# Kernel tuning notes

Measured on AMD Instinct MI355X. Metric: run time of the kernel, lower is better.

Reference implementation:

```python
import jax, jax.numpy as jnp
import numpy as np

SEQ_LEN = 256
NLAYERS = 3
H = 128  # latent_dim == input_dim
OUT_DIM = 2
BATCH = 1024


def setup_inputs() -> dict:
    key = jax.random.key(0)
    ks = jax.random.split(key, 7)
    s = 1.0 / np.sqrt(H)  # PyTorch RNN init scale
    return {
        "hiddens": jax.random.normal(ks[0], (BATCH, NLAYERS, H), jnp.float32),
        "W_ih": jax.random.uniform(ks[1], (NLAYERS, 3 * H, H), jnp.float32, -s, s),
        "W_hh": jax.random.uniform(ks[2], (NLAYERS, 3 * H, H), jnp.float32, -s, s),
        "b_ih": jax.random.uniform(ks[3], (NLAYERS, 3 * H), jnp.float32, -s, s),
        "b_hh": jax.random.uniform(ks[4], (NLAYERS, 3 * H), jnp.float32, -s, s),
        "fc_w": jax.random.uniform(ks[5], (OUT_DIM, H), jnp.float32, -s, s),
        "fc_b": jax.random.uniform(ks[6], (OUT_DIM,), jnp.float32, -s, s),
    }


def _gru_cell(x, h, w_ih, w_hh, bi, bh):
    # x, h: [B, H]; w_*: [3H, H]; b_*: [3H]; PyTorch gate order (r, z, n)
    gx = x @ w_ih.T + bi          # [B, 3H]
    gh = h @ w_hh.T + bh          # [B, 3H]
    xr, xz, xn = jnp.split(gx, 3, axis=-1)
    hr, hz, hn = jnp.split(gh, 3, axis=-1)
    r = jax.nn.sigmoid(xr + hr)
    z = jax.nn.sigmoid(xz + hz)
    n = jnp.tanh(xn + r * hn)
    return (1.0 - z) * n + z * h


def reference(hiddens, W_ih, W_hh, b_ih, b_hh, fc_w, fc_b):
    # hiddens: [B, L, H] -> layer-major [L, B, H] (torch transposes 0,1)
    h = jnp.transpose(hiddens, (1, 0, 2))
    B = hiddens.shape[0]
    x0 = jnp.zeros((B, H), hiddens.dtype)  # torch.zeros initial input

    def step(carry, _):
        x, h = carry
        new_h = []
        inp = x
        for l in range(NLAYERS):
            hl = _gru_cell(inp, h[l], W_ih[l], W_hh[l], b_ih[l], b_hh[l])
            new_h.append(hl)
            inp = hl  # top-layer output feeds next layer / next step
        return (inp, jnp.stack(new_h)), inp

    (_, _), outs = jax.lax.scan(step, (x0, h), None, length=SEQ_LEN)
    outs = jnp.transpose(outs, (1, 0, 2))        # [B, T, H]
    return outs @ fc_w.T + fc_b                  # [B, T, out_dim]
```

## Files before the change

kernel.cpp:

```cpp
#include <hip/hip_runtime.h>
#include <stdint.h>

typedef int   v4i __attribute__((ext_vector_type(4)));
typedef float v4f __attribute__((ext_vector_type(4)));

#define SLOT_SZ  13824
#define LO_OFF   6912
#define BIAS_OFF (2*SLOT_SZ)
#define FC_OFF   (BIAS_OFF + 6144)
#define SMEM_SZ  (FC_OFF + 2048)

#define QW   1436.84056f
#define C1f  4.38394754e-5f
#define C2f  3.45193507e-7f

__device__ __forceinline__ float sigm(float x) {
  return __builtin_amdgcn_rcpf(1.f + __expf(-x));
}
__device__ __forceinline__ float tanh_(float x) {
  return 1.f - 2.f * __builtin_amdgcn_rcpf(1.f + __expf(2.f * x));
}

__global__ void prep_weights(const float* __restrict__ Wih,
                             const float* __restrict__ Whh,
                             int8_t* __restrict__ img) {
  int bid = blockIdx.x, lane = threadIdx.x;
  int w = bid / 36, blk = bid % 36;
  int l = blk / 12, rem = blk % 12, o = rem >> 1, kh = rem & 1;
  const float* M = (o & 1) ? Whh : Wih;
  int row = (o >> 1) * 128 + w * 16 + (lane & 15);
  int k0 = kh * 64 + (lane >> 4) * 16;
  const float* src = M + l * 49152 + row * 128 + k0;
  int words[4];
  #pragma unroll
  for (int j4 = 0; j4 < 4; ++j4) {
    unsigned wd = 0;
    #pragma unroll
    for (int j = 0; j < 4; ++j) {
      int q = (int)rintf(src[j4 * 4 + j] * QW);
      wd |= ((unsigned)(q & 255)) << (8 * j);
    }
    words[j4] = (int)wd;
  }
  *(v4i*)(img + (((long)bid) * 64 + lane) * 16) = *(const v4i*)words;
}

__device__ __forceinline__ unsigned pack_hi(const float* f, const float* fhi) {
  unsigned wd = 0;
  #pragma unroll
  for (int r = 0; r < 4; ++r) {
    int v = (int)fhi[r];
    wd |= ((unsigned)(v & 255)) << (8 * r);
  }
  return wd;
}

__global__ __launch_bounds__(512, 2)
void gru_main(const float* __restrict__ hiddens, const float* __restrict__ bih,
              const float* __restrict__ bhh, const float* __restrict__ fcw,
              const float* __restrict__ fcb, const int8_t* __restrict__ img,
              float* __restrict__ out) {
  extern __shared__ char smem[];
  const int tid = threadIdx.x, wg = blockIdx.x;
  const int lane = tid & 63, w = tid >> 6, col = lane & 15, q = lane >> 4;

  v4i wr[36];
  #pragma unroll
  for (int i = 0; i < 36; ++i)
    wr[i] = *(const v4i*)(img + (((long)(w * 36 + i)) * 64 + lane) * 16);

  if (tid < 128) {
    int kh = tid >> 6, ln = tid & 63, c2 = ln & 15, q2 = ln >> 4;
    int words[4] = {0, 0, 0, 0};
    if (c2 < 2) {
      const float* src = fcw + c2 * 128 + kh * 64 + q2 * 16;
      #pragma unroll
      for (int j4 = 0; j4 < 4; ++j4) {
        unsigned wd = 0;
        #pragma unroll
        for (int j = 0; j < 4; ++j) {
          int qv = (int)rintf(src[j4 * 4 + j] * QW);
          wd |= ((unsigned)(qv & 255)) << (8 * j);
        }
        words[j4] = (int)wd;
      }
    }
    *(v4i*)(smem + FC_OFF + kh * 1024 + ln * 16) = *(const v4i*)words;
  }
  for (int i = tid; i < 1536; i += 512) {
    int l = i >> 9, type = (i >> 7) & 3, h = i & 127;
    float bv;
    if      (type == 0) bv = bih[l * 384 + h]       + bhh[l * 384 + h];
    else if (type == 1) bv = bih[l * 384 + 128 + h] + bhh[l * 384 + 128 + h];
    else if (type == 2) bv = bih[l * 384 + 256 + h];
    else                bv = bhh[l * 384 + 256 + h];
    *(float*)(smem + BIAS_OFF + i * 4) = bv;
  }
  for (int i = tid; i < 6144; i += 512) {
    int l = i >> 11, b = (i >> 7) & 15, h = i & 127;
    float v = hiddens[((long)(wg * 16 + b)) * 384 + l * 128 + h];
    float f = v * 15.875f, fhi = rintf(f);
    *(int8_t*)(smem + l * 2304 + b * 144 + h)          = (int8_t)(int)fhi;
    *(int8_t*)(smem + l * 2304 + b * 144 + h + LO_OFF) = (int8_t)(int)rintf((f - fhi) * 127.f);
  }
  v4f hst[3];
  #pragma unroll
  for (int l = 0; l < 3; ++l)
    #pragma unroll
    for (int r = 0; r < 4; ++r)
      hst[l][r] = hiddens[((long)(wg * 16 + col)) * 384 + l * 128 + w * 16 + q * 4 + r];

  const float fcb0 = fcb[0], fcb1 = fcb[1];
  __syncthreads();

  const char* fragb = smem + col * 144 + q * 16;
  char* ewb = smem + col * 144 + w * 16 + q * 4;
  const char* biasb = smem + BIAS_OFF + (w * 16 + q * 4) * 4;

  v4i c2h[2], c2l[2];

  #pragma unroll 1
  for (int t = 0; t < 256; ++t) {
    const int so = (t & 1) * SLOT_SZ;
    const int sn = SLOT_SZ - so;
    #pragma unroll
    for (int l = 0; l < 3; ++l) {
      v4i aRh = {0,0,0,0}, aRl = {0,0,0,0}, aZh = {0,0,0,0}, aZl = {0,0,0,0};
      v4i aXh = {0,0,0,0}, aXl = {0,0,0,0}, aHh = {0,0,0,0}, aHl = {0,0,0,0};
      if (l > 0 || t > 0) {
        #pragma unroll
        for (int kh = 0; kh < 2; ++kh) {
          v4i xh, xl;
          if (l == 0) {
            xh = *(const v4i*)(fragb + so + 2 * 2304 + kh * 64);
            xl = *(const v4i*)(fragb + so + 2 * 2304 + kh * 64 + LO_OFF);
            c2h[kh] = xh; c2l[kh] = xl;
          } else {
            xh = *(const v4i*)(fragb + sn + (l - 1) * 2304 + kh * 64);
            xl = *(const v4i*)(fragb + sn + (l - 1) * 2304 + kh * 64 + LO_OFF);
          }
          aRh = __builtin_amdgcn_mfma_i32_16x16x64_i8(wr[l*12 + 0 + kh], xh, aRh, 0, 0, 0);
          aRl = __builtin_amdgcn_mfma_i32_16x16x64_i8(wr[l*12 + 0 + kh], xl, aRl, 0, 0, 0);
          aZh = __builtin_amdgcn_mfma_i32_16x16x64_i8(wr[l*12 + 4 + kh], xh, aZh, 0, 0, 0);
          aZl = __builtin_amdgcn_mfma_i32_16x16x64_i8(wr[l*12 + 4 + kh], xl, aZl, 0, 0, 0);
          aXh = __builtin_amdgcn_mfma_i32_16x16x64_i8(wr[l*12 + 8 + kh], xh, aXh, 0, 0, 0);
          aXl = __builtin_amdgcn_mfma_i32_16x16x64_i8(wr[l*12 + 8 + kh], xl, aXl, 0, 0, 0);
        }
      }
      #pragma unroll
      for (int kh = 0; kh < 2; ++kh) {
        v4i hh, hl;
        if (l == 2) {
          if (t == 0) { c2h[kh] = *(const v4i*)(fragb + so + 2 * 2304 + kh * 64);
                        c2l[kh] = *(const v4i*)(fragb + so + 2 * 2304 + kh * 64 + LO_OFF); }
          hh = c2h[kh]; hl = c2l[kh];
        } else {
          hh = *(const v4i*)(fragb + so + l * 2304 + kh * 64);
          hl = *(const v4i*)(fragb + so + l * 2304 + kh * 64 + LO_OFF);
        }
        aRh = __builtin_amdgcn_mfma_i32_16x16x64_i8(wr[l*12 + 2 + kh], hh, aRh, 0, 0, 0);
        aRl = __builtin_amdgcn_mfma_i32_16x16x64_i8(wr[l*12 + 2 + kh], hl, aRl, 0, 0, 0);
        aZh = __builtin_amdgcn_mfma_i32_16x16x64_i8(wr[l*12 + 6 + kh], hh, aZh, 0, 0, 0);
        aZl = __builtin_amdgcn_mfma_i32_16x16x64_i8(wr[l*12 + 6 + kh], hl, aZl, 0, 0, 0);
        aHh = __builtin_amdgcn_mfma_i32_16x16x64_i8(wr[l*12 + 10 + kh], hh, aHh, 0, 0, 0);
        aHl = __builtin_amdgcn_mfma_i32_16x16x64_i8(wr[l*12 + 10 + kh], hl, aHl, 0, 0, 0);
      }
      v4f bRv = *(const v4f*)(biasb + (l * 4 + 0) * 512);
      v4f bZv = *(const v4f*)(biasb + (l * 4 + 1) * 512);
      v4f bXv = *(const v4f*)(biasb + (l * 4 + 2) * 512);
      v4f bHv = *(const v4f*)(biasb + (l * 4 + 3) * 512);
      unsigned hiw = 0, low = 0;
      #pragma unroll
      for (int r = 0; r < 4; ++r) {
        float gR = bRv[r] + C1f * (float)aRh[r] + C2f * (float)aRl[r];
        float gZ = bZv[r] + C1f * (float)aZh[r] + C2f * (float)aZl[r];
        float gX = bXv[r] + C1f * (float)aXh[r] + C2f * (float)aXl[r];
        float gH = bHv[r] + C1f * (float)aHh[r] + C2f * (float)aHl[r];
        float rg = sigm(gR), zg = sigm(gZ);
        float ng = tanh_(gX + rg * gH);
        float hn = ng + zg * (hst[l][r] - ng);
        hst[l][r] = hn;
        float f = hn * 15.875f, fhi = rintf(f);
        hiw |= ((unsigned)(((int)fhi) & 255)) << (8 * r);
        low |= ((unsigned)(((int)rintf((f - fhi) * 127.f)) & 255)) << (8 * r);
      }
      *(unsigned*)(ewb + sn + l * 2304)          = hiw;
      *(unsigned*)(ewb + sn + l * 2304 + LO_OFF) = low;
      __syncthreads();
    }
    if (w == 0) {
      v4i dh = {0,0,0,0}, dl = {0,0,0,0};
      #pragma unroll
      for (int kh = 0; kh < 2; ++kh) {
        v4i xh = *(const v4i*)(fragb + sn + 2 * 2304 + kh * 64);
        v4i xl = *(const v4i*)(fragb + sn + 2 * 2304 + kh * 64 + LO_OFF);
        v4i fw = *(const v4i*)(smem + FC_OFF + kh * 1024 + lane * 16);
        dh = __builtin_amdgcn_mfma_i32_16x16x64_i8(fw, xh, dh, 0, 0, 0);
        dl = __builtin_amdgcn_mfma_i32_16x16x64_i8(fw, xl, dl, 0, 0, 0);
      }
      if (q == 0) {
        float2 o2;
        o2.x = fcb0 + C1f * (float)dh[0] + C2f * (float)dl[0];
        o2.y = fcb1 + C1f * (float)dh[1] + C2f * (float)dl[1];
        *(float2*)(out + (((long)(wg * 16 + col)) * 256 + t) * 2) = o2;
      }
    }
  }
}

extern "C" void kernel_launch(void* const* d_in, const int* in_sizes, int n_in,
                              void* d_out, int out_size, void* d_ws, size_t ws_size,
                              hipStream_t stream) {
  (void)in_sizes; (void)n_in; (void)out_size; (void)ws_size;
  const float* hiddens = (const float*)d_in[0];
  const float* Wih     = (const float*)d_in[1];
  const float* Whh     = (const float*)d_in[2];
  const float* bih     = (const float*)d_in[3];
  const float* bhh     = (const float*)d_in[4];
  const float* fcw     = (const float*)d_in[5];
  const float* fcb     = (const float*)d_in[6];
  int8_t* img = (int8_t*)d_ws;
  float* out = (float*)d_out;

  prep_weights<<<288, 64, 0, stream>>>(Wih, Whh, img);
  gru_main<<<64, 512, SMEM_SZ, stream>>>(hiddens, bih, bhh, fcw, fcb, img, out);
}
```

Baseline: 900.6 us.

## Defer FC projection into next step's layer-0 phase and issue recurrent MFMAs first

Moves the wave-0 FC output projection for step t-1 into step t's layer-0 block, where it reuses the already-loaded top-layer fragments. This removes the serial FC tail that previously ran after the last barrier of each step. The final step's output is written after the loop from slot 0. Each layer now loads all operands up front and issues the hidden-state MFMAs before the input MFMAs, so MFMA work can start while input fragments arrive. The cost is more code to maintain and a new epilogue whose correctness depends on the slot parity of the final step.

```diff
diff --git a/kernel.cpp b/kernel.cpp
--- a/kernel.cpp
+++ b/kernel.cpp
@@ -45,15 +45,21 @@
   *(v4i*)(img + (((long)bid) * 64 + lane) * 16) = *(const v4i*)words;
 }
 
-__device__ __forceinline__ unsigned pack_hi(const float* f, const float* fhi) {
-  unsigned wd = 0;
-  #pragma unroll
-  for (int r = 0; r < 4; ++r) {
-    int v = (int)fhi[r];
-    wd |= ((unsigned)(v & 255)) << (8 * r);
-  }
-  return wd;
-}
+#define MFMA8(kh, Ah, Al, base)                                                \
+  aRh = __builtin_amdgcn_mfma_i32_16x16x64_i8(wr[(base) + 0 + (kh)], Ah, aRh, 0, 0, 0); \
+  aRl = __builtin_amdgcn_mfma_i32_16x16x64_i8(wr[(base) + 0 + (kh)], Al, aRl, 0, 0, 0); \
+  aZh = __builtin_amdgcn_mfma_i32_16x16x64_i8(wr[(base) + 4 + (kh)], Ah, aZh, 0, 0, 0); \
+  aZl = __builtin_amdgcn_mfma_i32_16x16x64_i8(wr[(base) + 4 + (kh)], Al, aZl, 0, 0, 0);
+
+#define MFMAX(kh, Ah, Al, base)                                                \
+  MFMA8(kh, Ah, Al, base)                                                      \
+  aXh = __builtin_amdgcn_mfma_i32_16x16x64_i8(wr[(base) + 8 + (kh)], Ah, aXh, 0, 0, 0); \
+  aXl = __builtin_amdgcn_mfma_i32_16x16x64_i8(wr[(base) + 8 + (kh)], Al, aXl, 0, 0, 0);
+
+#define MFMAH(kh, Ah, Al, base)                                                \
+  MFMA8(kh, Ah, Al, (base) + 2)                                                \
+  aHh = __builtin_amdgcn_mfma_i32_16x16x64_i8(wr[(base) + 10 + (kh)], Ah, aHh, 0, 0, 0); \
+  aHl = __builtin_amdgcn_mfma_i32_16x16x64_i8(wr[(base) + 10 + (kh)], Al, aHl, 0, 0, 0);
 
 __global__ __launch_bounds__(512, 2)
 void gru_main(const float* __restrict__ hiddens, const float* __restrict__ bih,
@@ -117,93 +123,122 @@
   char* ewb = smem + col * 144 + w * 16 + q * 4;
   const char* biasb = smem + BIAS_OFF + (w * 16 + q * 4) * 4;
 
-  v4i c2h[2], c2l[2];
+#define EW_STORE(l)                                                            \
+  {                                                                            \
+    v4f bRv = *(const v4f*)(biasb + ((l) * 4 + 0) * 512);                      \
+    v4f bZv = *(const v4f*)(biasb + ((l) * 4 + 1) * 512);                      \
+    v4f bXv = *(const v4f*)(biasb + ((l) * 4 + 2) * 512);                      \
+    v4f bHv = *(const v4f*)(biasb + ((l) * 4 + 3) * 512);                      \
+    unsigned hiw = 0, low = 0;                                                 \
+    _Pragma("unroll")                                                          \
+    for (int r = 0; r < 4; ++r) {                                              \
+      float gR = bRv[r] + C1f * (float)aRh[r] + C2f * (float)aRl[r];           \
+      float gZ = bZv[r] + C1f * (float)aZh[r] + C2f * (float)aZl[r];           \
+      float gX = bXv[r] + C1f * (float)aXh[r] + C2f * (float)aXl[r];           \
+      float gH = bHv[r] + C1f * (float)aHh[r] + C2f * (float)aHl[r];           \
+      float rg = sigm(gR), zg = sigm(gZ);                                      \
+      float ng = tanh_(gX + rg * gH);                                          \
+      float hn = ng + zg * (hst[l][r] - ng);                                   \
+      hst[l][r] = hn;                                                          \
+      float f = hn * 15.875f, fhi = rintf(f);                                  \
+      hiw |= ((unsigned)(((int)fhi) & 255)) << (8 * r);                        \
+      low |= ((unsigned)(((int)rintf((f - fhi) * 127.f)) & 255)) << (8 * r);   \
+    }                                                                          \
+    *(unsigned*)(ewb + sn + (l) * 2304)          = hiw;                        \
+    *(unsigned*)(ewb + sn + (l) * 2304 + LO_OFF) = low;                        \
+  }
 
   #pragma unroll 1
   for (int t = 0; t < 256; ++t) {
     const int so = (t & 1) * SLOT_SZ;
     const int sn = SLOT_SZ - so;
-    #pragma unroll
-    for (int l = 0; l < 3; ++l) {
+
+    {
+      v4i xh0[2], xl0[2], hh[2], hl[2];
+      #pragma unroll
+      for (int kh = 0; kh < 2; ++kh) {
+        xh0[kh] = *(const v4i*)(fragb + so + 2 * 2304 + kh * 64);
+        xl0[kh] = *(const v4i*)(fragb + so + 2 * 2304 + kh * 64 + LO_OFF);
+        hh[kh]  = *(const v4i*)(fragb + so + kh * 64);
+        hl[kh]  = *(const v4i*)(fragb + so + kh * 64 + LO_OFF);
+      }
       v4i aRh = {0,0,0,0}, aRl = {0,0,0,0}, aZh = {0,0,0,0}, aZl = {0,0,0,0};
       v4i aXh = {0,0,0,0}, aXl = {0,0,0,0}, aHh = {0,0,0,0}, aHl = {0,0,0,0};
-      if (l > 0 || t > 0) {
+      #pragma unroll
+      for (int kh = 0; kh < 2; ++kh) { MFMAH(kh, hh[kh], hl[kh], 0) }
+      if (t > 0) {
         #pragma unroll
-        for (int kh = 0; kh < 2; ++kh) {
-          v4i xh, xl;
-          if (l == 0) {
-            xh = *(const v4i*)(fragb + so + 2 * 2304 + kh * 64);
-            xl = *(const v4i*)(fragb + so + 2 * 2304 + kh * 64 + LO_OFF);
-            c2h[kh] = xh; c2l[kh] = xl;
-          } else {
-            xh = *(const v4i*)(fragb + sn + (l - 1) * 2304 + kh * 64);
-            xl = *(const v4i*)(fragb + sn + (l - 1) * 2304 + kh * 64 + LO_OFF);
+        for (int kh = 0; kh < 2; ++kh) { MFMAX(kh, xh0[kh], xl0[kh], 0) }
+        if (w == 0) {
+          v4i dh = {0,0,0,0}, dl = {0,0,0,0};
+          #pragma unroll
+          for (int kh = 0; kh < 2; ++kh) {
+            v4i fw = *(const v4i*)(smem + FC_OFF + kh * 1024 + lane * 16);
+            dh = __builtin_amdgcn_mfma_i32_16x16x64_i8(fw, xh0[kh], dh, 0, 0, 0);
+            dl = __builtin_amdgcn_mfma_i32_16x16x64_i8(fw, xl0[kh], dl, 0, 0, 0);
           }
-          aRh = __builtin_amdgcn_mfma_i32_16x16x64_i8(wr[l*12 + 0 + kh], xh, aRh, 0, 0, 0);
-          aRl = __builtin_amdgcn_mfma_i32_16x16x64_i8(wr[l*12 + 0 + kh], xl, aRl, 0, 0, 0);
-          aZh = __builtin_amdgcn_mfma_i32_16x16x64_i8(wr[l*12 + 4 + kh], xh, aZh, 0, 0, 0);
-          aZl = __builtin_amdgcn_mfma_i32_16x16x64_i8(wr[l*12 + 4 + kh], xl, aZl, 0, 0, 0);
-          aXh = __builtin_amdgcn_mfma_i32_16x16x64_i8(wr[l*12 + 8 + kh], xh, aXh, 0, 0, 0);
-          aXl = __builtin_amdgcn_mfma_i32_16x16x64_i8(wr[l*12 + 8 + kh], xl, aXl, 0, 0, 0);
+          if (q == 0) {
+            float2 o2;
+            o2.x = fcb0 + C1f * (float)dh[0] + C2f * (float)dl[0];
+            o2.y = fcb1 + C1f * (float)dh[1] + C2f * (float)dl[1];
+            *(float2*)(out + (((long)(wg * 16 + col)) * 256 + (t - 1)) * 2) = o2;
+          }
         }
       }
+      EW_STORE(0)
+    }
+    __syncthreads();
+
+    {
+      v4i xh[2], xl[2], hh[2], hl[2];
       #pragma unroll
       for (int kh = 0; kh < 2; ++kh) {
-        v4i hh, hl;
-        if (l == 2) {
-          if (t == 0) { c2h[kh] = *(const v4i*)(fragb + so + 2 * 2304 + kh * 64);
-                        c2l[kh] = *(const v4i*)(fragb + so + 2 * 2304 + kh * 64 + LO_OFF); }
-          hh = c2h[kh]; hl = c2l[kh];
-        } else {
-          hh = *(const v4i*)(fragb + so + l * 2304 + kh * 64);
-          hl = *(const v4i*)(fragb + so + l * 2304 + kh * 64 + LO_OFF);
-        }
-        aRh = __builtin_amdgcn_mfma_i32_16x16x64_i8(wr[l*12 + 2 + kh], hh, aRh, 0, 0, 0);
-        aRl = __builtin_amdgcn_mfma_i32_16x16x64_i8(wr[l*12 + 2 + kh], hl, aRl, 0, 0, 0);
-        aZh = __builtin_amdgcn_mfma_i32_16x16x64_i8(wr[l*12 + 6 + kh], hh, aZh, 0, 0, 0);
-        aZl = __builtin_amdgcn_mfma_i32_16x16x64_i8(wr[l*12 + 6 + kh], hl, aZl, 0, 0, 0);
-        aHh = __builtin_amdgcn_mfma_i32_16x16x64_i8(wr[l*12 + 10 + kh], hh, aHh, 0, 0, 0);
-        aHl = __builtin_amdgcn_mfma_i32_16x16x64_i8(wr[l*12 + 10 + kh], hl, aHl, 0, 0, 0);
-      }
-      v4f bRv = *(const v4f*)(biasb + (l * 4 + 0) * 512);
-      v4f bZv = *(const v4f*)(biasb + (l * 4 + 1) * 512);
-      v4f bXv = *(const v4f*)(biasb + (l * 4 + 2) * 512);
-      v4f bHv = *(const v4f*)(biasb + (l * 4 + 3) * 512);
-      unsigned hiw = 0, low = 0;
-      #pragma unroll
-      for (int r = 0; r < 4; ++r) {
-        float gR = bRv[r] + C1f * (float)aRh[r] + C2f * (float)aRl[r];
-        float gZ = bZv[r] + C1f * (float)aZh[r] + C2f * (float)aZl[r];
-        float gX = bXv[r] + C1f * (float)aXh[r] + C2f * (float)aXl[r];
-        float gH = bHv[r] + C1f * (float)aHh[r] + C2f * (float)aHl[r];
-        float rg = sigm(gR), zg = sigm(gZ);
-        float ng = tanh_(gX + rg * gH);
-        float hn = ng + zg * (hst[l][r] - ng);
-        hst[l][r] = hn;
-        float f = hn * 15.875f, fhi = rintf(f);
-        hiw |= ((unsigned)(((int)fhi) & 255)) << (8 * r);
-        low |= ((unsigned)(((int)rintf((f - fhi) * 127.f)) & 255)) << (8 * r);
-      }
-      *(unsigned*)(ewb + sn + l * 2304)          = hiw;
-      *(unsigned*)(ewb + sn + l * 2304 + LO_OFF) = low;
-      __syncthreads();
-    }
-    if (w == 0) {
-      v4i dh = {0,0,0,0}, dl = {0,0,0,0};
+        xh[kh] = *(const v4i*)(fragb + sn + kh * 64);
+        xl[kh] = *(const v4i*)(fragb + sn + kh * 64 + LO_OFF);
+        hh[kh] = *(const v4i*)(fragb + so + 1 * 2304 + kh * 64);
+        hl[kh] = *(const v4i*)(fragb + so + 1 * 2304 + kh * 64 + LO_OFF);
+      }
+      v4i aRh = {0,0,0,0}, aRl = {0,0,0,0}, aZh = {0,0,0,0}, aZl = {0,0,0,0};
+      v4i aXh = {0,0,0,0}, aXl = {0,0,0,0}, aHh = {0,0,0,0}, aHl = {0,0,0,0};
+      #pragma unroll
+      for (int kh = 0; kh < 2; ++kh) { MFMAH(kh, hh[kh], hl[kh], 12) MFMAX(kh, xh[kh], xl[kh], 12) }
+      EW_STORE(1)
+    }
+    __syncthreads();
+
+    {
+      v4i xh[2], xl[2], hh[2], hl[2];
       #pragma unroll
       for (int kh = 0; kh < 2; ++kh) {
-        v4i xh = *(const v4i*)(fragb + sn + 2 * 2304 + kh * 64);
-        v4i xl = *(const v4i*)(fragb + sn + 2 * 2304 + kh * 64 + LO_OFF);
-        v4i fw = *(const v4i*)(smem + FC_OFF + kh * 1024 + lane * 16);
-        dh = __builtin_amdgcn_mfma_i32_16x16x64_i8(fw, xh, dh, 0, 0, 0);
-        dl = __builtin_amdgcn_mfma_i32_16x16x64_i8(fw, xl, dl, 0, 0, 0);
-      }
-      if (q == 0) {
-        float2 o2;
-        o2.x = fcb0 + C1f * (float)dh[0] + C2f * (float)dl[0];
-        o2.y = fcb1 + C1f * (float)dh[1] + C2f * (float)dl[1];
-        *(float2*)(out + (((long)(wg * 16 + col)) * 256 + t) * 2) = o2;
-      }
+        xh[kh] = *(const v4i*)(fragb + sn + 1 * 2304 + kh * 64);
+        xl[kh] = *(const v4i*)(fragb + sn + 1 * 2304 + kh * 64 + LO_OFF);
+        hh[kh] = *(const v4i*)(fragb + so + 2 * 2304 + kh * 64);
+        hl[kh] = *(const v4i*)(fragb + so + 2 * 2304 + kh * 64 + LO_OFF);
+      }
+      v4i aRh = {0,0,0,0}, aRl = {0,0,0,0}, aZh = {0,0,0,0}, aZl = {0,0,0,0};
+      v4i aXh = {0,0,0,0}, aXl = {0,0,0,0}, aHh = {0,0,0,0}, aHl = {0,0,0,0};
+      #pragma unroll
+      for (int kh = 0; kh < 2; ++kh) { MFMAH(kh, hh[kh], hl[kh], 24) MFMAX(kh, xh[kh], xl[kh], 24) }
+      EW_STORE(2)
+    }
+    __syncthreads();
+  }
+
+  if (w == 0) {
+    v4i dh = {0,0,0,0}, dl = {0,0,0,0};
+    #pragma unroll
+    for (int kh = 0; kh < 2; ++kh) {
+      v4i xh = *(const v4i*)(fragb + 2 * 2304 + kh * 64);
+      v4i xl = *(const v4i*)(fragb + 2 * 2304 + kh * 64 + LO_OFF);
+      v4i fw = *(const v4i*)(smem + FC_OFF + kh * 1024 + lane * 16);
+      dh = __builtin_amdgcn_mfma_i32_16x16x64_i8(fw, xh, dh, 0, 0, 0);
+      dl = __builtin_amdgcn_mfma_i32_16x16x64_i8(fw, xl, dl, 0, 0, 0);
+    }
+    if (q == 0) {
+      float2 o2;
+      o2.x = fcb0 + C1f * (float)dh[0] + C2f * (float)dl[0];
+      o2.y = fcb1 + C1f * (float)dh[1] + C2f * (float)dl[1];
+      *(float2*)(out + (((long)(wg * 16 + col)) * 256 + 255) * 2) = o2;
     }
   }
 }
```

After: 909.0 us. About the same (+0.9%).

## Software-pipeline recurrent h-matmuls across phases and move n-gate weights to LDS

Applied to the files above, without the earlier changes.

The per-layer loop is restructured so that the recurrent W_hh matmul for the next layer's state is issued in the same phase as the current layer's input matmul and elementwise update. Accumulators ping-pong between two register sets, which shortens the serial chain between barriers. The n-gate W_hh weight fragments move from registers to LDS to free VGPRs. The FC output projection is spread across waves and merged into the phases, and the time loop is unrolled by two so buffer offsets become constants. The cost is extra LDS reads per phase, a larger shared-memory footprint that needs an attribute call, and much more complex code.

```diff
diff --git a/kernel.cpp b/kernel.cpp
--- a/kernel.cpp
+++ b/kernel.cpp
@@ -8,11 +8,14 @@
 #define LO_OFF   6912
 #define BIAS_OFF (2*SLOT_SZ)
 #define FC_OFF   (BIAS_OFF + 6144)
-#define SMEM_SZ  (FC_OFF + 2048)
+#define WLDS_OFF (FC_OFF + 2048)
+#define SMEM_SZ  (WLDS_OFF + 49152)
 
 #define QW   1436.84056f
 #define C1f  4.38394754e-5f
 #define C2f  3.45193507e-7f
+
+#define MFMA(A,B,C) __builtin_amdgcn_mfma_i32_16x16x64_i8(A, B, C, 0, 0, 0)
 
 __device__ __forceinline__ float sigm(float x) {
   return __builtin_amdgcn_rcpf(1.f + __expf(-x));
@@ -45,16 +48,6 @@
   *(v4i*)(img + (((long)bid) * 64 + lane) * 16) = *(const v4i*)words;
 }
 
-__device__ __forceinline__ unsigned pack_hi(const float* f, const float* fhi) {
-  unsigned wd = 0;
-  #pragma unroll
-  for (int r = 0; r < 4; ++r) {
-    int v = (int)fhi[r];
-    wd |= ((unsigned)(v & 255)) << (8 * r);
-  }
-  return wd;
-}
-
 __global__ __launch_bounds__(512, 2)
 void gru_main(const float* __restrict__ hiddens, const float* __restrict__ bih,
               const float* __restrict__ bhh, const float* __restrict__ fcw,
@@ -64,11 +57,18 @@
   const int tid = threadIdx.x, wg = blockIdx.x;
   const int lane = tid & 63, w = tid >> 6, col = lane & 15, q = lane >> 4;
 
-  v4i wr[36];
-  #pragma unroll
-  for (int i = 0; i < 36; ++i)
-    wr[i] = *(const v4i*)(img + (((long)(w * 36 + i)) * 64 + lane) * 16);
-
+  v4i wr[30];
+  #pragma unroll
+  for (int i = 0; i < 30; ++i) {
+    int blk = (i / 10) * 12 + (i % 10);
+    wr[i] = *(const v4i*)(img + (((long)(w * 36 + blk)) * 64 + lane) * 16);
+  }
+  #pragma unroll
+  for (int j = 0; j < 6; ++j) {
+    int blk = (j >> 1) * 12 + 10 + (j & 1);
+    *(v4i*)(smem + WLDS_OFF + w * 6144 + j * 1024 + lane * 16) =
+        *(const v4i*)(img + (((long)(w * 36 + blk)) * 64 + lane) * 16);
+  }
   if (tid < 128) {
     int kh = tid >> 6, ln = tid & 63, c2 = ln & 15, q2 = ln >> 4;
     int words[4] = {0, 0, 0, 0};
@@ -116,94 +116,155 @@
   const char* fragb = smem + col * 144 + q * 16;
   char* ewb = smem + col * 144 + w * 16 + q * 4;
   const char* biasb = smem + BIAS_OFF + (w * 16 + q * 4) * 4;
-
-  v4i c2h[2], c2l[2];
+  const char* wldsp = smem + WLDS_OFF + w * 6144 + lane * 16;
+
+#define FC_BLOCK(FCT, XOFF) { \
+  if (w == ((FCT) & 3)) { \
+    v4i dh = {0,0,0,0}, dl = {0,0,0,0}; \
+    _Pragma("unroll") \
+    for (int kh = 0; kh < 2; ++kh) { \
+      v4i fxh = *(const v4i*)(fragb + (XOFF) + kh * 64); \
+      v4i fxl = *(const v4i*)(fragb + (XOFF) + kh * 64 + LO_OFF); \
+      v4i fw  = *(const v4i*)(smem + FC_OFF + kh * 1024 + lane * 16); \
+      dh = MFMA(fw, fxh, dh); dl = MFMA(fw, fxl, dl); } \
+    if (q == 0) { float2 o2; \
+      o2.x = fcb0 + C1f * (float)dh[0] + C2f * (float)dl[0]; \
+      o2.y = fcb1 + C1f * (float)dh[1] + C2f * (float)dl[1]; \
+      *(float2*)(out + (((long)(wg * 16 + col)) * 256 + ((FCT) - 1)) * 2) = o2; } } }
+
+#define EW_STORE(L, WOFF, Rh, Rl, Zh, Zl, Xh, Xl, Hh, Hl) { \
+  v4f bRv = *(const v4f*)(biasb + ((L) * 4 + 0) * 512); \
+  v4f bZv = *(const v4f*)(biasb + ((L) * 4 + 1) * 512); \
+  v4f bXv = *(const v4f*)(biasb + ((L) * 4 + 2) * 512); \
+  v4f bHv = *(const v4f*)(biasb + ((L) * 4 + 3) * 512); \
+  unsigned hiw = 0, low = 0; \
+  _Pragma("unroll") \
+  for (int r = 0; r < 4; ++r) { \
+    float gR = bRv[r] + C1f * (float)Rh[r] + C2f * (float)Rl[r]; \
+    float gZ = bZv[r] + C1f * (float)Zh[r] + C2f * (float)Zl[r]; \
+    float gX = bXv[r] + C1f * (float)Xh[r] + C2f * (float)Xl[r]; \
+    float gH = bHv[r] + C1f * (float)Hh[r] + C2f * (float)Hl[r]; \
+    float rg = sigm(gR), zg = sigm(gZ); \
+    float ng = tanh_(gX + rg * gH); \
+    float hn = ng + zg * (hst[L][r] - ng); \
+    hst[L][r] = hn; \
+    float f = hn * 15.875f, fhi = rintf(f); \
+    hiw |= ((unsigned)(((int)fhi) & 255)) << (8 * r); \
+    low |= ((unsigned)(((int)rintf((f - fhi) * 127.f)) & 255)) << (8 * r); } \
+  *(unsigned*)(ewb + (WOFF)) = hiw; \
+  *(unsigned*)(ewb + (WOFF) + LO_OFF) = low; }
+
+#define PHASE(L, XV, XOFF, HV, HL, HOFF, cRh,cRl,cZh,cZl,cHh,cHl, \
+              nRh,nRl,nZh,nZl,nHh,nHl, WOFF, FCV, FCT) { \
+  v4i Xh = {0,0,0,0}, Xl = {0,0,0,0}; \
+  if (XV) { \
+    v4i xh0 = *(const v4i*)(fragb + (XOFF)); \
+    v4i xh1 = *(const v4i*)(fragb + (XOFF) + 64); \
+    v4i xl0 = *(const v4i*)(fragb + (XOFF) + LO_OFF); \
+    v4i xl1 = *(const v4i*)(fragb + (XOFF) + LO_OFF + 64); \
+    cRh = MFMA(wr[(L)*10+0], xh0, cRh); cRh = MFMA(wr[(L)*10+1], xh1, cRh); \
+    cRl = MFMA(wr[(L)*10+0], xl0, cRl); cRl = MFMA(wr[(L)*10+1], xl1, cRl); \
+    cZh = MFMA(wr[(L)*10+4], xh0, cZh); cZh = MFMA(wr[(L)*10+5], xh1, cZh); \
+    cZl = MFMA(wr[(L)*10+4], xl0, cZl); cZl = MFMA(wr[(L)*10+5], xl1, cZl); \
+    Xh  = MFMA(wr[(L)*10+8], xh0, Xh);  Xh  = MFMA(wr[(L)*10+9], xh1, Xh); \
+    Xl  = MFMA(wr[(L)*10+8], xl0, Xl);  Xl  = MFMA(wr[(L)*10+9], xl1, Xl); \
+    if (FCV) FC_BLOCK(FCT, XOFF) \
+  } \
+  nRh = (v4i){0,0,0,0}; nRl = (v4i){0,0,0,0}; nZh = (v4i){0,0,0,0}; \
+  nZl = (v4i){0,0,0,0}; nHh = (v4i){0,0,0,0}; nHl = (v4i){0,0,0,0}; \
+  if (HV) { \
+    v4i hh0 = *(const v4i*)(fragb + (HOFF)); \
+    v4i hh1 = *(const v4i*)(fragb + (HOFF) + 64); \
+    v4i hl0 = *(const v4i*)(fragb + (HOFF) + LO_OFF); \
+    v4i hl1 = *(const v4i*)(fragb + (HOFF) + LO_OFF + 64); \
+    v4i wn0 = *(const v4i*)(wldsp + (HL) * 2048); \
+    v4i wn1 = *(const v4i*)(wldsp + (HL) * 2048 + 1024); \
+    nRh = MFMA(wr[(HL)*10+2], hh0, nRh); nRh = MFMA(wr[(HL)*10+3], hh1, nRh); \
+    nRl = MFMA(wr[(HL)*10+2], hl0, nRl); nRl = MFMA(wr[(HL)*10+3], hl1, nRl); \
+    nZh = MFMA(wr[(HL)*10+6], hh0, nZh); nZh = MFMA(wr[(HL)*10+7], hh1, nZh); \
+    nZl = MFMA(wr[(HL)*10+6], hl0, nZl); nZl = MFMA(wr[(HL)*10+7], hl1, nZl); \
+    nHh = MFMA(wn0, hh0, nHh); nHh = MFMA(wn1, hh1, nHh); \
+    nHl = MFMA(wn0, hl0, nHl); nHl = MFMA(wn1, hl1, nHl); \
+  } \
+  EW_STORE(L, WOFF, cRh, cRl, cZh, cZl, Xh, Xl, cHh, cHl) \
+  __syncthreads(); }
+
+  v4i A_Rh, A_Rl, A_Zh, A_Zl, A_Hh, A_Hl;
+  v4i B_Rh, B_Rl, B_Zh, B_Zl, B_Hh, B_Hl;
+
+  {
+    A_Rh = (v4i){0,0,0,0}; A_Rl = (v4i){0,0,0,0}; A_Zh = (v4i){0,0,0,0};
+    A_Zl = (v4i){0,0,0,0}; A_Hh = (v4i){0,0,0,0}; A_Hl = (v4i){0,0,0,0};
+    v4i hh0 = *(const v4i*)(fragb + 0);
+    v4i hh1 = *(const v4i*)(fragb + 64);
+    v4i hl0 = *(const v4i*)(fragb + LO_OFF);
+    v4i hl1 = *(const v4i*)(fragb + LO_OFF + 64);
+    v4i wn0 = *(const v4i*)(wldsp + 0);
+    v4i wn1 = *(const v4i*)(wldsp + 1024);
+    A_Rh = MFMA(wr[2], hh0, A_Rh); A_Rh = MFMA(wr[3], hh1, A_Rh);
+    A_Rl = MFMA(wr[2], hl0, A_Rl); A_Rl = MFMA(wr[3], hl1, A_Rl);
+    A_Zh = MFMA(wr[6], hh0, A_Zh); A_Zh = MFMA(wr[7], hh1, A_Zh);
+    A_Zl = MFMA(wr[6], hl0, A_Zl); A_Zl = MFMA(wr[7], hl1, A_Zl);
+    A_Hh = MFMA(wn0, hh0, A_Hh);   A_Hh = MFMA(wn1, hh1, A_Hh);
+    A_Hl = MFMA(wn0, hl0, A_Hl);   A_Hl = MFMA(wn1, hl1, A_Hl);
+  }
+  PHASE(0, 0, 0, 1, 1, 1*2304,
+        A_Rh,A_Rl,A_Zh,A_Zl,A_Hh,A_Hl, B_Rh,B_Rl,B_Zh,B_Zl,B_Hh,B_Hl,
+        SLOT_SZ + 0, 0, 0)
+  PHASE(1, 1, SLOT_SZ + 0, 1, 2, 2*2304,
+        B_Rh,B_Rl,B_Zh,B_Zl,B_Hh,B_Hl, A_Rh,A_Rl,A_Zh,A_Zl,A_Hh,A_Hl,
+        SLOT_SZ + 1*2304, 0, 0)
+  PHASE(2, 1, SLOT_SZ + 1*2304, 1, 0, SLOT_SZ + 0,
+        A_Rh,A_Rl,A_Zh,A_Zl,A_Hh,A_Hl, B_Rh,B_Rl,B_Zh,B_Zl,B_Hh,B_Hl,
+        SLOT_SZ + 2*2304, 0, 0)
 
   #pragma unroll 1
-  for (int t = 0; t < 256; ++t) {
-    const int so = (t & 1) * SLOT_SZ;
-    const int sn = SLOT_SZ - so;
+  for (int ti = 0; ti < 127; ++ti) {
+    const int T = 2 * ti + 1;
+    PHASE(0, 1, SLOT_SZ + 2*2304, 1, 1, SLOT_SZ + 1*2304,
+          B_Rh,B_Rl,B_Zh,B_Zl,B_Hh,B_Hl, A_Rh,A_Rl,A_Zh,A_Zl,A_Hh,A_Hl,
+          0, 1, T)
+    PHASE(1, 1, 0, 1, 2, SLOT_SZ + 2*2304,
+          A_Rh,A_Rl,A_Zh,A_Zl,A_Hh,A_Hl, B_Rh,B_Rl,B_Zh,B_Zl,B_Hh,B_Hl,
+          1*2304, 0, 0)
+    PHASE(2, 1, 1*2304, 1, 0, 0,
+          B_Rh,B_Rl,B_Zh,B_Zl,B_Hh,B_Hl, A_Rh,A_Rl,A_Zh,A_Zl,A_Hh,A_Hl,
+          2*2304, 0, 0)
+    PHASE(0, 1, 2*2304, 1, 1, 1*2304,
+          A_Rh,A_Rl,A_Zh,A_Zl,A_Hh,A_Hl, B_Rh,B_Rl,B_Zh,B_Zl,B_Hh,B_Hl,
+          SLOT_SZ + 0, 1, T + 1)
+    PHASE(1, 1, SLOT_SZ + 0, 1, 2, 2*2304,
+          B_Rh,B_Rl,B_Zh,B_Zl,B_Hh,B_Hl, A_Rh,A_Rl,A_Zh,A_Zl,A_Hh,A_Hl,
+          SLOT_SZ + 1*2304, 0, 0)
+    PHASE(2, 1, SLOT_SZ + 1*2304, 1, 0, SLOT_SZ + 0,
+          A_Rh,A_Rl,A_Zh,A_Zl,A_Hh,A_Hl, B_Rh,B_Rl,B_Zh,B_Zl,B_Hh,B_Hl,
+          SLOT_SZ + 2*2304, 0, 0)
+  }
+
+  PHASE(0, 1, SLOT_SZ + 2*2304, 1, 1, SLOT_SZ + 1*2304,
+        B_Rh,B_Rl,B_Zh,B_Zl,B_Hh,B_Hl, A_Rh,A_Rl,A_Zh,A_Zl,A_Hh,A_Hl,
+        0, 1, 255)
+  PHASE(1, 1, 0, 1, 2, SLOT_SZ + 2*2304,
+        A_Rh,A_Rl,A_Zh,A_Zl,A_Hh,A_Hl, B_Rh,B_Rl,B_Zh,B_Zl,B_Hh,B_Hl,
+        1*2304, 0, 0)
+  PHASE(2, 1, 1*2304, 0, 0, 0,
+        B_Rh,B_Rl,B_Zh,B_Zl,B_Hh,B_Hl, A_Rh,A_Rl,A_Zh,A_Zl,A_Hh,A_Hl,
+        2*2304, 0, 0)
+
+  if (w == 0) {
+    v4i dh = {0,0,0,0}, dl = {0,0,0,0};
     #pragma unroll
-    for (int l = 0; l < 3; ++l) {
-      v4i aRh = {0,0,0,0}, aRl = {0,0,0,0}, aZh = {0,0,0,0}, aZl = {0,0,0,0};
-      v4i aXh = {0,0,0,0}, aXl = {0,0,0,0}, aHh = {0,0,0,0}, aHl = {0,0,0,0};
-      if (l > 0 || t > 0) {
-        #pragma unroll
-        for (int kh = 0; kh < 2; ++kh) {
-          v4i xh, xl;
-          if (l == 0) {
-            xh = *(const v4i*)(fragb + so + 2 * 2304 + kh * 64);
-            xl = *(const v4i*)(fragb + so + 2 * 2304 + kh * 64 + LO_OFF);
-            c2h[kh] = xh; c2l[kh] = xl;
-          } else {
-            xh = *(const v4i*)(fragb + sn + (l - 1) * 2304 + kh * 64);
-            xl = *(const v4i*)(fragb + sn + (l - 1) * 2304 + kh * 64 + LO_OFF);
-          }
-          aRh = __builtin_amdgcn_mfma_i32_16x16x64_i8(wr[l*12 + 0 + kh], xh, aRh, 0, 0, 0);
-          aRl = __builtin_amdgcn_mfma_i32_16x16x64_i8(wr[l*12 + 0 + kh], xl, aRl, 0, 0, 0);
-          aZh = __builtin_amdgcn_mfma_i32_16x16x64_i8(wr[l*12 + 4 + kh], xh, aZh, 0, 0, 0);
-          aZl = __builtin_amdgcn_mfma_i32_16x16x64_i8(wr[l*12 + 4 + kh], xl, aZl, 0, 0, 0);
-          aXh = __builtin_amdgcn_mfma_i32_16x16x64_i8(wr[l*12 + 8 + kh], xh, aXh, 0, 0, 0);
-          aXl = __builtin_amdgcn_mfma_i32_16x16x64_i8(wr[l*12 + 8 + kh], xl, aXl, 0, 0, 0);
-        }
-      }
-      #pragma unroll
-      for (int kh = 0; kh < 2; ++kh) {
-        v4i hh, hl;
-        if (l == 2) {
-          if (t == 0) { c2h[kh] = *(const v4i*)(fragb + so + 2 * 2304 + kh * 64);
-                        c2l[kh] = *(const v4i*)(fragb + so + 2 * 2304 + kh * 64 + LO_OFF); }
-          hh = c2h[kh]; hl = c2l[kh];
-        } else {
-          hh = *(const v4i*)(fragb + so + l * 2304 + kh * 64);
-          hl = *(const v4i*)(fragb + so + l * 2304 + kh * 64 + LO_OFF);
-        }
-        aRh = __builtin_amdgcn_mfma_i32_16x16x64_i8(wr[l*12 + 2 + kh], hh, aRh, 0, 0, 0);
-        aRl = __builtin_amdgcn_mfma_i32_16x16x64_i8(wr[l*12 + 2 + kh], hl, aRl, 0, 0, 0);
-        aZh = __builtin_amdgcn_mfma_i32_16x16x64_i8(wr[l*12 + 6 + kh], hh, aZh, 0, 0, 0);
-        aZl = __builtin_amdgcn_mfma_i32_16x16x64_i8(wr[l*12 + 6 + kh], hl, aZl, 0, 0, 0);
-        aHh = __builtin_amdgcn_mfma_i32_16x16x64_i8(wr[l*12 + 10 + kh], hh, aHh, 0, 0, 0);
-        aHl = __builtin_amdgcn_mfma_i32_16x16x64_i8(wr[l*12 + 10 + kh], hl, aHl, 0, 0, 0);
-      }
-      v4f bRv = *(const v4f*)(biasb + (l * 4 + 0) * 512);
-      v4f bZv = *(const v4f*)(biasb + (l * 4 + 1) * 512);
-      v4f bXv = *(const v4f*)(biasb + (l * 4 + 2) * 512);
-      v4f bHv = *(const v4f*)(biasb + (l * 4 + 3) * 512);
-      unsigned hiw = 0, low = 0;
-      #pragma unroll
-      for (int r = 0; r < 4; ++r) {
-        float gR = bRv[r] + C1f * (float)aRh[r] + C2f * (float)aRl[r];
-        float gZ = bZv[r] + C1f * (float)aZh[r] + C2f * (float)aZl[r];
-        float gX = bXv[r] + C1f * (float)aXh[r] + C2f * (float)aXl[r];
-        float gH = bHv[r] + C1f * (float)aHh[r] + C2f * (float)aHl[r];
-        float rg = sigm(gR), zg = sigm(gZ);
-        float ng = tanh_(gX + rg * gH);
-        float hn = ng + zg * (hst[l][r] - ng);
-        hst[l][r] = hn;
-        float f = hn * 15.875f, fhi = rintf(f);
-        hiw |= ((unsigned)(((int)fhi) & 255)) << (8 * r);
-        low |= ((unsigned)(((int)rintf((f - fhi) * 127.f)) & 255)) << (8 * r);
-      }
-      *(unsigned*)(ewb + sn + l * 2304)          = hiw;
-      *(unsigned*)(ewb + sn + l * 2304 + LO_OFF) = low;
-      __syncthreads();
-    }
-    if (w == 0) {
-      v4i dh = {0,0,0,0}, dl = {0,0,0,0};
-      #pragma unroll
-      for (int kh = 0; kh < 2; ++kh) {
-        v4i xh = *(const v4i*)(fragb + sn + 2 * 2304 + kh * 64);
-        v4i xl = *(const v4i*)(fragb + sn + 2 * 2304 + kh * 64 + LO_OFF);
-        v4i fw = *(const v4i*)(smem + FC_OFF + kh * 1024 + lane * 16);
-        dh = __builtin_amdgcn_mfma_i32_16x16x64_i8(fw, xh, dh, 0, 0, 0);
-        dl = __builtin_amdgcn_mfma_i32_16x16x64_i8(fw, xl, dl, 0, 0, 0);
-      }
-      if (q == 0) {
-        float2 o2;
-        o2.x = fcb0 + C1f * (float)dh[0] + C2f * (float)dl[0];
-        o2.y = fcb1 + C1f * (float)dh[1] + C2f * (float)dl[1];
-        *(float2*)(out + (((long)(wg * 16 + col)) * 256 + t) * 2) = o2;
-      }
+    for (int kh = 0; kh < 2; ++kh) {
+      v4i fxh = *(const v4i*)(fragb + 2*2304 + kh * 64);
+      v4i fxl = *(const v4i*)(fragb + 2*2304 + kh * 64 + LO_OFF);
+      v4i fw  = *(const v4i*)(smem + FC_OFF + kh * 1024 + lane * 16);
+      dh = MFMA(fw, fxh, dh); dl = MFMA(fw, fxl, dl);
+    }
+    if (q == 0) {
+      float2 o2;
+      o2.x = fcb0 + C1f * (float)dh[0] + C2f * (float)dl[0];
+      o2.y = fcb1 + C1f * (float)dh[1] + C2f * (float)dl[1];
+      *(float2*)(out + (((long)(wg * 16 + col)) * 256 + 255) * 2) = o2;
     }
   }
 }
@@ -222,6 +283,9 @@
   int8_t* img = (int8_t*)d_ws;
   float* out = (float*)d_out;
 
+  hipFuncSetAttribute(reinterpret_cast<const void*>(gru_main),
+                      hipFuncAttributeMaxDynamicSharedMemorySize, SMEM_SZ);
+
   prep_weights<<<288, 64, 0, stream>>>(Wih, Whh, img);
   gru_main<<<64, 512, SMEM_SZ, stream>>>(hiddens, bih, bhh, fcw, fcb, img, out);
 }
```

Result: no change. 915.7 us (+1.7%).
